# Performance work log

Measured on AMD Instinct MI355X. Metric: run time of the kernel, lower is better.

## Reference

```python
import jax, jax.numpy as jnp
import numpy as np

N_NODES = 50000
N_EDGES = 500000
NODE_DIM = 128
EDGE_DIM = 64
OUT_DIM = 128


def setup_inputs() -> dict:
    key = jax.random.key(0)
    k1, k2, k3, k4, k5, k6 = jax.random.split(key, 6)
    node_feats = jax.random.normal(k1, (N_NODES, NODE_DIM), dtype=jnp.float32)
    edge_feats = jax.random.normal(k2, (N_EDGES, EDGE_DIM), dtype=jnp.float32)
    src_idx = jax.random.randint(k3, (N_EDGES,), 0, N_NODES, dtype=jnp.int32)
    dst_idx = jax.random.randint(k4, (N_EDGES,), 0, N_NODES, dtype=jnp.int32)
    in_dim = 2 * NODE_DIM + EDGE_DIM
    # nn.Linear-style init scale
    scale = 1.0 / np.sqrt(in_dim)
    W = jax.random.normal(k5, (in_dim, OUT_DIM), dtype=jnp.float32) * scale
    b = jax.random.normal(k6, (OUT_DIM,), dtype=jnp.float32) * scale
    return {"node_feats": node_feats, "edge_feats": edge_feats,
            "src_idx": src_idx, "dst_idx": dst_idx, "W": W, "b": b}


def reference(node_feats, edge_feats, src_idx, dst_idx, W, b):
    # Gather per-edge src/dst node features, concat with edge feats (residual=True)
    src = node_feats[src_idx]            # [E, node_dim]
    dst = node_feats[dst_idx]            # [E, node_dim]
    combined = jnp.concatenate([src, dst, edge_feats], axis=-1)  # [E, 2*nd+ed]
    score = combined @ W + b             # [E, out_dim]
    return score
```

## Files before the change

kernel.cpp:

```cpp
#include <hip/hip_runtime.h>
#include <hip/hip_bf16.h>
#include <cstdint>

#define N_NODES 50000
#define N_EDGES 500000
#define ND 128
#define ED 64
#define OD 128

typedef __attribute__((ext_vector_type(8))) short short8;
typedef __attribute__((ext_vector_type(4))) float f32x4;
typedef unsigned long long u64;

__device__ __forceinline__ unsigned short f2bf(float f) {
    union { float f; unsigned u; } c; c.f = f;
    unsigned u = c.u;
    unsigned r = (u + 0x7FFFu + ((u >> 16) & 1u)) >> 16;
    return (unsigned short)r;
}
__device__ __forceinline__ float bf2f(unsigned short s) {
    union { unsigned u; float f; } c; c.u = ((unsigned)s) << 16;
    return c.f;
}

__device__ __forceinline__ void store_u64_agent(u64* p, u64 v) {
    __hip_atomic_store(p, v, __ATOMIC_RELAXED, __HIP_MEMORY_SCOPE_AGENT);
}
__device__ __forceinline__ u64 load_u64_agent(const u64* p) {
    return __hip_atomic_load(const_cast<u64*>(p), __ATOMIC_RELAXED, __HIP_MEMORY_SCOPE_AGENT);
}

__global__ void prep_kernel(const float* __restrict__ W,
                            u64* __restrict__ wbtNP64,
                            u64* __restrict__ wbtE64) {
    int g = blockIdx.x * 256 + threadIdx.x;
    if (g < 8192) {
        int n = g >> 5, k0 = (g & 31) * 4;
        u64 v = 0;
#pragma unroll
        for (int j = 0; j < 4; ++j) {
            int k = k0 + j;
            float f = (n < 128) ? W[k * OD + n] : W[(128 + k) * OD + (n - 128)];
            v |= ((u64)f2bf(f)) << (16 * j);
        }
        store_u64_agent(wbtNP64 + g, v);
    } else if (g < 10240) {
        int h = g - 8192;
        int n = h >> 4, k0 = (h & 15) * 4;
        u64 v = 0;
#pragma unroll
        for (int j = 0; j < 4; ++j) {
            int k = k0 + j;
            v |= ((u64)f2bf(W[(256 + k) * OD + n])) << (16 * j);
        }
        store_u64_agent(wbtE64 + h, v);
    }
}

__launch_bounds__(256)
__global__ void nodeproj_kernel(const float* __restrict__ nf,
                                const u64* __restrict__ wbtNP64,
                                u64* __restrict__ P64) {
    __shared__ char lds[16384 + 65536];
    int tid = threadIdx.x;
    int m0 = blockIdx.x * 64;

#pragma unroll
    for (int i = 0; i < 8; ++i) {
        int idx = tid + i * 256;
        int row = idx >> 5, c4 = idx & 31;
        int m = m0 + row;
        float4 v = make_float4(0.f, 0.f, 0.f, 0.f);
        if (m < N_NODES) v = *(const float4*)(nf + m * ND + c4 * 4);
        uint2 pk;
        pk.x = (unsigned)f2bf(v.x) | ((unsigned)f2bf(v.y) << 16);
        pk.y = (unsigned)f2bf(v.z) | ((unsigned)f2bf(v.w) << 16);
        int byte = (row * 256 + c4 * 8) ^ ((row & 7) << 4);
        *(uint2*)(lds + byte) = pk;
    }
#pragma unroll
    for (int i = 0; i < 32; ++i) {
        int idx = tid + i * 256;
        int row = idx >> 5, c4 = idx & 31;
        u64 v = load_u64_agent(wbtNP64 + row * 32 + c4);
        int byte = 16384 + ((row * 256 + c4 * 8) ^ ((row & 7) << 4));
        *(u64*)(lds + byte) = v;
    }
    __syncthreads();

    int lane = tid & 63, wid = tid >> 6;
    f32x4 acc[16];
#pragma unroll
    for (int i = 0; i < 16; ++i) acc[i] = (f32x4){0.f, 0.f, 0.f, 0.f};

    int mrow = 16 * wid + (lane & 15);
    int abase = mrow * 256;
    int aswz = (mrow & 7) << 4;
#pragma unroll
    for (int kc = 0; kc < 4; ++kc) {
        int kb = kc * 64 + ((lane >> 4) << 4);
        short8 nfr = *(const short8*)(lds + ((abase + kb) ^ aswz));
#pragma unroll
        for (int mt = 0; mt < 16; ++mt) {
            int n = 16 * mt + (lane & 15);
            short8 w = *(const short8*)(lds + 16384 + ((n * 256 + kb) ^ ((n & 7) << 4)));
            acc[mt] = __builtin_amdgcn_mfma_f32_16x16x32_bf16(w, nfr, acc[mt], 0, 0, 0);
        }
    }

    int m = m0 + mrow;
    if (m < N_NODES) {
        int lg = lane >> 4;
        u64* Prow = P64 + (size_t)m * 64;
#pragma unroll
        for (int mt = 0; mt < 16; ++mt) {
            unsigned lo = (unsigned)f2bf(acc[mt][0]) | ((unsigned)f2bf(acc[mt][1]) << 16);
            unsigned hi = (unsigned)f2bf(acc[mt][2]) | ((unsigned)f2bf(acc[mt][3]) << 16);
            store_u64_agent(Prow + mt * 4 + lg, (u64)lo | ((u64)hi << 32));
        }
    }
}

__launch_bounds__(256)
__global__ void edge_kernel(const float* __restrict__ ef,
                            const int* __restrict__ src,
                            const int* __restrict__ dst,
                            const u64* __restrict__ wbtE64,
                            const u64* __restrict__ P64,
                            const float* __restrict__ bias,
                            float* __restrict__ out) {
    __shared__ char lds[8192 + 16384];
    int tid = threadIdx.x;
    int e0 = blockIdx.x * 64;

#pragma unroll
    for (int i = 0; i < 4; ++i) {
        int idx = tid + i * 256;
        int row = idx >> 4, c4 = idx & 15;
        int e = e0 + row;
        float4 v = make_float4(0.f, 0.f, 0.f, 0.f);
        if (e < N_EDGES) v = *(const float4*)(ef + e * ED + c4 * 4);
        uint2 pk;
        pk.x = (unsigned)f2bf(v.x) | ((unsigned)f2bf(v.y) << 16);
        pk.y = (unsigned)f2bf(v.z) | ((unsigned)f2bf(v.w) << 16);
        int byte = (row * 128 + c4 * 8) ^ ((row & 7) << 4);
        *(uint2*)(lds + byte) = pk;
    }
#pragma unroll
    for (int i = 0; i < 8; ++i) {
        int idx = tid + i * 256;
        int row = idx >> 4, c4 = idx & 15;
        u64 v = load_u64_agent(wbtE64 + row * 16 + c4);
        int byte = 8192 + ((row * 128 + c4 * 8) ^ ((row & 7) << 4));
        *(u64*)(lds + byte) = v;
    }
    __syncthreads();

    int lane = tid & 63, wid = tid >> 6, lg = lane >> 4;
    f32x4 acc[8];
#pragma unroll
    for (int i = 0; i < 8; ++i) acc[i] = (f32x4){0.f, 0.f, 0.f, 0.f};

    int erow = 16 * wid + (lane & 15);
    int ebase = erow * 128;
    int eswz = (erow & 7) << 4;
#pragma unroll
    for (int kc = 0; kc < 2; ++kc) {
        int kb = kc * 64 + (lg << 4);
        short8 efr = *(const short8*)(lds + ((ebase + kb) ^ eswz));
#pragma unroll
        for (int mt = 0; mt < 8; ++mt) {
            int n = 16 * mt + (lane & 15);
            short8 w = *(const short8*)(lds + 8192 + ((n * 128 + kb) ^ ((n & 7) << 4)));
            acc[mt] = __builtin_amdgcn_mfma_f32_16x16x32_bf16(w, efr, acc[mt], 0, 0, 0);
        }
    }

    int e = e0 + erow;
    bool ok = e < N_EDGES;
    int ec = ok ? e : (N_EDGES - 1);
    int s = src[ec], d = dst[ec];
    const u64* Ps = P64 + (size_t)s * 64;
    const u64* Pd = P64 + (size_t)d * 64 + 32;
    u64 g1[8], g2[8];
#pragma unroll
    for (int mt = 0; mt < 8; ++mt) {
        g1[mt] = load_u64_agent(Ps + mt * 4 + lg);
        g2[mt] = load_u64_agent(Pd + mt * 4 + lg);
    }
    float* orow = out + (size_t)e * OD + 4 * lg;
#pragma unroll
    for (int mt = 0; mt < 8; ++mt) {
        float4 bv = *(const float4*)(bias + 16 * mt + 4 * lg);
        unsigned p1x = (unsigned)g1[mt], p1y = (unsigned)(g1[mt] >> 32);
        unsigned p2x = (unsigned)g2[mt], p2y = (unsigned)(g2[mt] >> 32);
        float4 o;
        o.x = acc[mt][0] + bv.x + bf2f((unsigned short)(p1x & 0xFFFF)) + bf2f((unsigned short)(p2x & 0xFFFF));
        o.y = acc[mt][1] + bv.y + bf2f((unsigned short)(p1x >> 16))    + bf2f((unsigned short)(p2x >> 16));
        o.z = acc[mt][2] + bv.z + bf2f((unsigned short)(p1y & 0xFFFF)) + bf2f((unsigned short)(p2y & 0xFFFF));
        o.w = acc[mt][3] + bv.w + bf2f((unsigned short)(p1y >> 16))    + bf2f((unsigned short)(p2y >> 16));
        if (ok) *(float4*)(orow + 16 * mt) = o;
    }
}

__global__ void naive_kernel(const float* __restrict__ nf, const float* __restrict__ ef,
                             const int* __restrict__ src, const int* __restrict__ dst,
                             const float* __restrict__ W, const float* __restrict__ bias,
                             float* __restrict__ out) {
    long g = (long)blockIdx.x * 256 + threadIdx.x;
    if (g >= (long)N_EDGES * OD) return;
    int e = (int)(g >> 7), j = (int)(g & 127);
    int s = src[e], d = dst[e];
    float sum = bias[j];
    for (int k = 0; k < ND; ++k) sum += nf[s * ND + k] * W[k * OD + j];
    for (int k = 0; k < ND; ++k) sum += nf[d * ND + k] * W[(ND + k) * OD + j];
    for (int k = 0; k < ED; ++k) sum += ef[e * ED + k] * W[(2 * ND + k) * OD + j];
    out[g] = sum;
}

extern "C" void kernel_launch(void* const* d_in, const int* in_sizes, int n_in,
                              void* d_out, int out_size, void* d_ws, size_t ws_size,
                              hipStream_t stream) {
    const float* nf  = (const float*)d_in[0];
    const float* ef  = (const float*)d_in[1];
    const int*   src = (const int*)d_in[2];
    const int*   dst = (const int*)d_in[3];
    const float* W   = (const float*)d_in[4];
    const float* bias= (const float*)d_in[5];
    float* out = (float*)d_out;

    const size_t need = 65536 + 16384 + (size_t)N_NODES * 512;
    if (ws_size < need) {
        long total = (long)N_EDGES * OD;
        naive_kernel<<<(int)((total + 255) / 256), 256, 0, stream>>>(nf, ef, src, dst, W, bias, out);
        return;
    }
    u64* wbtNP64 = (u64*)d_ws;
    u64* wbtE64  = (u64*)((char*)d_ws + 65536);
    u64* P64     = (u64*)((char*)d_ws + 81920);

    prep_kernel<<<40, 256, 0, stream>>>(W, wbtNP64, wbtE64);
    nodeproj_kernel<<<(N_NODES + 63) / 64, 256, 0, stream>>>(nf, wbtNP64, P64);
    edge_kernel<<<(N_EDGES + 63) / 64, 256, 0, stream>>>(ef, src, dst, wbtE64, P64, bias, out);
}
```

Baseline: 495.7 us.

## Fuse weight prep into projection and edge kernels, load edge feats directly

Removes the separate weight-conversion kernel. Each block of the node projection and edge kernels now converts its slice of W from fp32 to bf16 straight into LDS. The edge kernel drops the LDS staging of edge features and reads them per lane into MFMA fragments. It also issues the src/dst gathers before the barrier so they overlap with the weight staging. This saves a launch and some LDS traffic, at the cost of redundant strided W reads and conversions in every block (7800+ edge blocks) and scalar 2-byte LDS stores.

```diff
diff --git a/kernel.cpp b/kernel.cpp
--- a/kernel.cpp
+++ b/kernel.cpp
@@ -30,36 +30,9 @@
     return __hip_atomic_load(const_cast<u64*>(p), __ATOMIC_RELAXED, __HIP_MEMORY_SCOPE_AGENT);
 }
 
-__global__ void prep_kernel(const float* __restrict__ W,
-                            u64* __restrict__ wbtNP64,
-                            u64* __restrict__ wbtE64) {
-    int g = blockIdx.x * 256 + threadIdx.x;
-    if (g < 8192) {
-        int n = g >> 5, k0 = (g & 31) * 4;
-        u64 v = 0;
-#pragma unroll
-        for (int j = 0; j < 4; ++j) {
-            int k = k0 + j;
-            float f = (n < 128) ? W[k * OD + n] : W[(128 + k) * OD + (n - 128)];
-            v |= ((u64)f2bf(f)) << (16 * j);
-        }
-        store_u64_agent(wbtNP64 + g, v);
-    } else if (g < 10240) {
-        int h = g - 8192;
-        int n = h >> 4, k0 = (h & 15) * 4;
-        u64 v = 0;
-#pragma unroll
-        for (int j = 0; j < 4; ++j) {
-            int k = k0 + j;
-            v |= ((u64)f2bf(W[(256 + k) * OD + n])) << (16 * j);
-        }
-        store_u64_agent(wbtE64 + h, v);
-    }
-}
-
 __launch_bounds__(256)
 __global__ void nodeproj_kernel(const float* __restrict__ nf,
-                                const u64* __restrict__ wbtNP64,
+                                const float* __restrict__ W,
                                 u64* __restrict__ P64) {
     __shared__ char lds[16384 + 65536];
     int tid = threadIdx.x;
@@ -78,13 +51,15 @@
         int byte = (row * 256 + c4 * 8) ^ ((row & 7) << 4);
         *(uint2*)(lds + byte) = pk;
     }
-#pragma unroll
-    for (int i = 0; i < 32; ++i) {
-        int idx = tid + i * 256;
-        int row = idx >> 5, c4 = idx & 31;
-        u64 v = load_u64_agent(wbtNP64 + row * 32 + c4);
-        int byte = 16384 + ((row * 256 + c4 * 8) ^ ((row & 7) << 4));
-        *(u64*)(lds + byte) = v;
+    {
+        int n = tid;
+        const float* Wcol = (n < 128) ? (W + n) : (W + 128 * OD + (n - 128));
+        int rowb = 16384 + n * 256;
+        int swz = (n & 7) << 4;
+#pragma unroll 16
+        for (int k = 0; k < 128; ++k) {
+            *(unsigned short*)(lds + (((rowb + k * 2) ^ swz))) = f2bf(Wcol[(size_t)k * OD]);
+        }
     }
     __syncthreads();
 
@@ -125,61 +100,29 @@
 __global__ void edge_kernel(const float* __restrict__ ef,
                             const int* __restrict__ src,
                             const int* __restrict__ dst,
-                            const u64* __restrict__ wbtE64,
+                            const float* __restrict__ W,
                             const u64* __restrict__ P64,
                             const float* __restrict__ bias,
                             float* __restrict__ out) {
-    __shared__ char lds[8192 + 16384];
+    __shared__ char lds[16384];
     int tid = threadIdx.x;
     int e0 = blockIdx.x * 64;
-
-#pragma unroll
-    for (int i = 0; i < 4; ++i) {
-        int idx = tid + i * 256;
-        int row = idx >> 4, c4 = idx & 15;
-        int e = e0 + row;
-        float4 v = make_float4(0.f, 0.f, 0.f, 0.f);
-        if (e < N_EDGES) v = *(const float4*)(ef + e * ED + c4 * 4);
-        uint2 pk;
-        pk.x = (unsigned)f2bf(v.x) | ((unsigned)f2bf(v.y) << 16);
-        pk.y = (unsigned)f2bf(v.z) | ((unsigned)f2bf(v.w) << 16);
-        int byte = (row * 128 + c4 * 8) ^ ((row & 7) << 4);
-        *(uint2*)(lds + byte) = pk;
-    }
-#pragma unroll
-    for (int i = 0; i < 8; ++i) {
-        int idx = tid + i * 256;
-        int row = idx >> 4, c4 = idx & 15;
-        u64 v = load_u64_agent(wbtE64 + row * 16 + c4);
-        int byte = 8192 + ((row * 128 + c4 * 8) ^ ((row & 7) << 4));
-        *(u64*)(lds + byte) = v;
-    }
-    __syncthreads();
-
     int lane = tid & 63, wid = tid >> 6, lg = lane >> 4;
-    f32x4 acc[8];
-#pragma unroll
-    for (int i = 0; i < 8; ++i) acc[i] = (f32x4){0.f, 0.f, 0.f, 0.f};
 
     int erow = 16 * wid + (lane & 15);
-    int ebase = erow * 128;
-    int eswz = (erow & 7) << 4;
-#pragma unroll
-    for (int kc = 0; kc < 2; ++kc) {
-        int kb = kc * 64 + (lg << 4);
-        short8 efr = *(const short8*)(lds + ((ebase + kb) ^ eswz));
-#pragma unroll
-        for (int mt = 0; mt < 8; ++mt) {
-            int n = 16 * mt + (lane & 15);
-            short8 w = *(const short8*)(lds + 8192 + ((n * 128 + kb) ^ ((n & 7) << 4)));
-            acc[mt] = __builtin_amdgcn_mfma_f32_16x16x32_bf16(w, efr, acc[mt], 0, 0, 0);
-        }
-    }
-
     int e = e0 + erow;
     bool ok = e < N_EDGES;
     int ec = ok ? e : (N_EDGES - 1);
     int s = src[ec], d = dst[ec];
+
+#pragma unroll
+    for (int i = 0; i < 32; ++i) {
+        int idx = tid + i * 256;
+        int n = idx & 127, k = idx >> 7;
+        unsigned short b = f2bf(W[(size_t)(256 + k) * OD + n]);
+        *(unsigned short*)(lds + ((n * 128 + k * 2) ^ ((n & 7) << 4))) = b;
+    }
+
     const u64* Ps = P64 + (size_t)s * 64;
     const u64* Pd = P64 + (size_t)d * 64 + 32;
     u64 g1[8], g2[8];
@@ -188,6 +131,32 @@
         g1[mt] = load_u64_agent(Ps + mt * 4 + lg);
         g2[mt] = load_u64_agent(Pd + mt * 4 + lg);
     }
+
+    __syncthreads();
+
+    f32x4 acc[8];
+#pragma unroll
+    for (int i = 0; i < 8; ++i) acc[i] = (f32x4){0.f, 0.f, 0.f, 0.f};
+
+    const float* efrow = ef + (size_t)ec * ED;
+#pragma unroll
+    for (int kc = 0; kc < 2; ++kc) {
+        float4 f0 = *(const float4*)(efrow + kc * 32 + lg * 8);
+        float4 f1 = *(const float4*)(efrow + kc * 32 + lg * 8 + 4);
+        short8 efr;
+        efr[0] = (short)f2bf(f0.x); efr[1] = (short)f2bf(f0.y);
+        efr[2] = (short)f2bf(f0.z); efr[3] = (short)f2bf(f0.w);
+        efr[4] = (short)f2bf(f1.x); efr[5] = (short)f2bf(f1.y);
+        efr[6] = (short)f2bf(f1.z); efr[7] = (short)f2bf(f1.w);
+        int kb = kc * 64 + lg * 16;
+#pragma unroll
+        for (int mt = 0; mt < 8; ++mt) {
+            int n = 16 * mt + (lane & 15);
+            short8 w = *(const short8*)(lds + ((n * 128 + kb) ^ ((n & 7) << 4)));
+            acc[mt] = __builtin_amdgcn_mfma_f32_16x16x32_bf16(w, efr, acc[mt], 0, 0, 0);
+        }
+    }
+
     float* orow = out + (size_t)e * OD + 4 * lg;
 #pragma unroll
     for (int mt = 0; mt < 8; ++mt) {
@@ -229,17 +198,14 @@
     const float* bias= (const float*)d_in[5];
     float* out = (float*)d_out;
 
-    const size_t need = 65536 + 16384 + (size_t)N_NODES * 512;
+    const size_t need = (size_t)N_NODES * 512;
     if (ws_size < need) {
         long total = (long)N_EDGES * OD;
         naive_kernel<<<(int)((total + 255) / 256), 256, 0, stream>>>(nf, ef, src, dst, W, bias, out);
         return;
     }
-    u64* wbtNP64 = (u64*)d_ws;
-    u64* wbtE64  = (u64*)((char*)d_ws + 65536);
-    u64* P64     = (u64*)((char*)d_ws + 81920);
-
-    prep_kernel<<<40, 256, 0, stream>>>(W, wbtNP64, wbtE64);
-    nodeproj_kernel<<<(N_NODES + 63) / 64, 256, 0, stream>>>(nf, wbtNP64, P64);
-    edge_kernel<<<(N_EDGES + 63) / 64, 256, 0, stream>>>(ef, src, dst, wbtE64, P64, bias, out);
-}
+    u64* P64 = (u64*)d_ws;
+
+    nodeproj_kernel<<<(N_NODES + 63) / 64, 256, 0, stream>>>(nf, W, P64);
+    edge_kernel<<<(N_EDGES + 63) / 64, 256, 0, stream>>>(ef, src, dst, W, P64, bias, out);
+}
```

Result: faster. 477.6 us (-3.7%).
